# Kernel optimization log

Hardware: AMD Instinct MI355X
Metric: run time of the kernel (lower is better)

## Reference

```python
import jax, jax.numpy as jnp
import numpy as np

# Llama-2-7B-like GQA attention, prefill over packed equal-length sequences
H = 4096      # hidden_size
NH = 32       # num_attention_heads
NKV = 8       # num_key_value_heads
HD = H // NH  # head_dim = 128
B = 4         # number of packed sequences
S = 1024      # seq_len per sequence
T = B * S     # total packed tokens
BASE = 10000.0  # rope_theta


def setup_inputs() -> dict:
    key = jax.random.key(0)
    ks = jax.random.split(key, 5)
    x = jax.random.normal(ks[0], (T, H), jnp.float32)
    positions = jnp.tile(jnp.arange(S, dtype=jnp.int32), B)  # per-seq positions
    kv_cache = jnp.zeros((1,), jnp.float32)  # placeholder (prefill: kv from current tokens)
    init = 0.02
    wq = jax.random.normal(ks[1], (NH * HD, H), jnp.float32) * init
    wk = jax.random.normal(ks[2], (NKV * HD, H), jnp.float32) * init
    wv = jax.random.normal(ks[3], (NKV * HD, H), jnp.float32) * init
    wo = jax.random.normal(ks[4], (H, NH * HD), jnp.float32) * init
    return {"x": x, "positions": positions, "kv_cache": kv_cache,
            "wq": wq, "wk": wk, "wv": wv, "wo": wo, "seq_len": S}


def _rope(xh, cos_b, sin_b):
    # xh: [T, Hh, D]; cos_b/sin_b: [T, 1, D] (freqs repeat-interleaved by 2)
    half = xh.shape[-1] // 2
    x_rot = jnp.concatenate([-xh[..., half:], xh[..., :half]], axis=-1)
    return xh * cos_b + x_rot * sin_b


def reference(x, positions, kv_cache, wq, wk, wv, wo, seq_len):
    Tn = x.shape[0]
    q = (x @ wq.T).reshape(Tn, NH, HD)
    k = (x @ wk.T).reshape(Tn, NKV, HD)
    v = (x @ wv.T).reshape(Tn, NKV, HD)
    # GQA: repeat_interleave kv heads
    rep = NH // NKV
    k = jnp.repeat(k, rep, axis=1)
    v = jnp.repeat(v, rep, axis=1)
    # RoPE tables (faithful to _precompute_freqs/_rotary_embeddings)
    inv_freq = 1.0 / (BASE ** (jnp.arange(0, HD, 2, dtype=jnp.float32) / HD))
    t = jnp.arange(seq_len, dtype=jnp.float32)
    freqs = t[:, None] * inv_freq[None, :]            # [S, D/2]
    cos, sin = jnp.cos(freqs), jnp.sin(freqs)
    pos = jnp.clip(positions.astype(jnp.int32), 0, seq_len - 1)
    cos_b = jnp.repeat(cos[pos], 2, axis=-1)[:, None, :]  # [T,1,D]
    sin_b = jnp.repeat(sin[pos], 2, axis=-1)[:, None, :]
    q = _rope(q, cos_b, sin_b)
    k = _rope(k, cos_b, sin_b)
    # Paged attention (prefill): causal attention within each packed sequence
    Bn = Tn // seq_len
    qb = q.reshape(Bn, seq_len, NH, HD)
    kb = k.reshape(Bn, seq_len, NH, HD)
    vb = v.reshape(Bn, seq_len, NH, HD)
    scores = jnp.einsum('bqhd,bkhd->bhqk', qb, kb) * (HD ** -0.5)
    causal = jnp.tril(jnp.ones((seq_len, seq_len), bool))
    scores = jnp.where(causal[None, None], scores, -jnp.inf)
    probs = jax.nn.softmax(scores, axis=-1)
    out = jnp.einsum('bhqk,bkhd->bqhd', probs, vb).reshape(Tn, NH * HD)
    return out @ wo.T
```

## Files before the change

### kernel.cpp

```cpp
#include <hip/hip_runtime.h>
#include <hip/hip_bf16.h>
#include <math.h>

#define T_TOK 4096
#define HID   4096
#define NHQ   32
#define NKVH  8
#define HDIM  128
#define SEQ   1024
#define NBATCH 4

typedef __attribute__((ext_vector_type(8))) short bf16x8;
typedef __attribute__((ext_vector_type(4))) float f32x4;

__device__ __forceinline__ unsigned short f2bf(float f) {
  union { float f; unsigned int u; } x; x.f = f;
  unsigned int r = x.u + 0x7FFFu + ((x.u >> 16) & 1u);
  return (unsigned short)(r >> 16);
}

#define GLOAD_LDS16(gp, lp)                                                        \
  __builtin_amdgcn_global_load_lds(                                                \
      (__attribute__((address_space(1))) void*)(unsigned long long)(const void*)(gp), \
      (__attribute__((address_space(3))) void*)(unsigned long long)(const void*)(lp), \
      16, 0, 0)

__global__ __launch_bounds__(256) void cast_all_k(const float* __restrict__ x,
                                                  const float* __restrict__ wq,
                                                  const float* __restrict__ wk,
                                                  const float* __restrict__ wv,
                                                  const float* __restrict__ wo,
                                                  unsigned short* __restrict__ xb,
                                                  unsigned short* __restrict__ wqkv,
                                                  unsigned short* __restrict__ wob) {
  int i = blockIdx.x * 256 + threadIdx.x;
  const float* src; unsigned short* dst; int off;
  if (i < 4194304)       { src = x;  dst = xb;   off = i; }
  else if (i < 8388608)  { src = wq; dst = wqkv; off = i - 4194304; }
  else if (i < 9437184)  { src = wk; dst = wqkv + 16777216; off = i - 8388608; }
  else if (i < 10485760) { src = wv; dst = wqkv + 20971520; off = i - 9437184; }
  else                   { src = wo; dst = wob;  off = i - 10485760; }
  float4 f = ((const float4*)src)[off];
  ushort4 o;
  o.x = f2bf(f.x); o.y = f2bf(f.y); o.z = f2bf(f.z); o.w = f2bf(f.w);
  ((ushort4*)dst)[off] = o;
}

template<bool FUSED>
__global__ __launch_bounds__(512, 2) void gemm8(const unsigned short* __restrict__ A,
                                                const unsigned short* __restrict__ B,
                                                float* __restrict__ C,
                                                const int* __restrict__ pos,
                                                unsigned short* __restrict__ qr,
                                                unsigned short* __restrict__ kr,
                                                unsigned short* __restrict__ vbuf,
                                                int N, int K) {
  __shared__ unsigned short AL[2][16384];
  __shared__ unsigned short BL[4][8192];
  const int tid  = threadIdx.x;
  const int lane = tid & 63;
  const int wave = tid >> 6;
  const int m16  = lane & 15;
  const int quad = lane >> 4;
  const int wm   = wave >> 1;
  const int wn   = wave & 1;

  const int gx = gridDim.x;
  const int nwg = gx * gridDim.y;
  const int orig = blockIdx.y * gx + blockIdx.x;
  const int swz = (orig & 7) * (nwg >> 3) + (orig >> 3);
  const long rowBase = (long)(swz / gx) * 256;
  const long colBase = (long)(swz % gx) * 128;

  int aoff[2], boff[2];
#pragma unroll
  for (int ks = 0; ks < 2; ++ks) {
    int sx = ((ks * 4 + quad) ^ (m16 & 7)) * 8;
    aoff[ks] = (wm * 64 + m16) * 64 + sx;
    boff[ks] = (wn * 32 + m16) * 64 + sx;
  }

  const long Kl = K;
  const int sck = ((tid & 7) ^ ((tid >> 3) & 7)) * 8;
  const unsigned short* gA = A + (rowBase + (tid >> 3)) * Kl + sck;
  const unsigned short* gB = B + (colBase + (tid >> 3)) * Kl + sck;
  const int dofs = wave * 512;

#define STG_B(slot_, ko_) { GLOAD_LDS16(gB + (ko_),            &BL[slot_][dofs]);         \
                            GLOAD_LDS16(gB + (ko_) + 64 * Kl,  &BL[slot_][4096 + dofs]); }
#define STG_A(slot_, ko_) { GLOAD_LDS16(gA + (ko_),            &AL[slot_][dofs]);         \
                            GLOAD_LDS16(gA + (ko_) + 64 * Kl,  &AL[slot_][4096 + dofs]);  \
                            GLOAD_LDS16(gA + (ko_) + 128 * Kl, &AL[slot_][8192 + dofs]);  \
                            GLOAD_LDS16(gA + (ko_) + 192 * Kl, &AL[slot_][12288 + dofs]); }

  f32x4 acc[4][4] = {};

  STG_B(0, 0); STG_A(0, 0); STG_B(1, 64); STG_A(1, 64);
  asm volatile("s_waitcnt vmcnt(6)" ::: "memory");
  __builtin_amdgcn_s_barrier();

  for (int it = 0; it < 16; ++it) {
#pragma unroll
    for (int u = 0; u < 4; ++u) {
      const int X = it * 4 + u;
      const int kn = ((X + 2) & 63) << 6;
      bf16x8 af[4][2], bf01[2][2], bf23[2][2];

#pragma unroll
      for (int mf = 0; mf < 4; ++mf)
#pragma unroll
        for (int ks = 0; ks < 2; ++ks)
          af[mf][ks] = *(const bf16x8*)(&AL[u & 1][aoff[ks] + mf * 1024]);
#pragma unroll
      for (int nf = 0; nf < 2; ++nf)
#pragma unroll
        for (int ks = 0; ks < 2; ++ks)
          bf01[nf][ks] = *(const bf16x8*)(&BL[u][boff[ks] + nf * 1024]);
      STG_B((u + 2) & 3, kn);
      asm volatile("s_waitcnt lgkmcnt(8)" ::: "memory");
      __builtin_amdgcn_s_barrier();
      asm volatile("s_waitcnt lgkmcnt(0)" ::: "memory");
      __builtin_amdgcn_s_setprio(1);
#pragma unroll
      for (int mf = 0; mf < 4; ++mf)
#pragma unroll
        for (int nf = 0; nf < 2; ++nf)
#pragma unroll
          for (int ks = 0; ks < 2; ++ks)
            acc[mf][nf] = __builtin_amdgcn_mfma_f32_16x16x32_bf16(af[mf][ks], bf01[nf][ks], acc[mf][nf], 0, 0, 0);
      __builtin_amdgcn_s_setprio(0);
      __builtin_amdgcn_s_barrier();

#pragma unroll
      for (int nf = 0; nf < 2; ++nf)
#pragma unroll
        for (int ks = 0; ks < 2; ++ks)
          bf23[nf][ks] = *(const bf16x8*)(&BL[u][boff[ks] + nf * 1024 + 4096]);
      STG_A(u & 1, kn);
      __builtin_amdgcn_s_barrier();
      asm volatile("s_waitcnt lgkmcnt(0)" ::: "memory");
      __builtin_amdgcn_s_setprio(1);
#pragma unroll
      for (int mf = 0; mf < 4; ++mf)
#pragma unroll
        for (int nf = 0; nf < 2; ++nf)
#pragma unroll
          for (int ks = 0; ks < 2; ++ks)
            acc[mf][nf + 2] = __builtin_amdgcn_mfma_f32_16x16x32_bf16(af[mf][ks], bf23[nf][ks], acc[mf][nf + 2], 0, 0, 0);
      __builtin_amdgcn_s_setprio(0);
      asm volatile("s_waitcnt vmcnt(6)" ::: "memory");
      __builtin_amdgcn_s_barrier();
    }
  }

  if (!FUSED) {
#pragma unroll
    for (int mf = 0; mf < 4; ++mf)
#pragma unroll
      for (int nf = 0; nf < 4; ++nf) {
        long c = colBase + wn * 32 + (nf & 1) * 16 + (nf >> 1) * 64 + m16;
#pragma unroll
        for (int reg = 0; reg < 4; ++reg) {
          long row = rowBase + wm * 64 + mf * 16 + quad * 4 + reg;
          C[row * N + c] = acc[mf][nf][reg];
        }
      }
    return;
  }

  const int n0 = (int)colBase;
  unsigned short* dst;
  int rstride, colofs;
  bool dorope;
  if (n0 < 4096)       { dst = qr;   rstride = NHQ * HDIM;  colofs = n0;        dorope = true; }
  else if (n0 < 5120)  { dst = kr;   rstride = NKVH * HDIM; colofs = n0 - 4096; dorope = true; }
  else                 { dst = vbuf; rstride = NKVH * HDIM; colofs = n0 - 5120; dorope = false; }
  const float c0 = -13.287712379549449f / 64.0f;
  float fA[2], fB[2];
#pragma unroll
  for (int e = 0; e < 2; ++e) {
    int d = wn * 32 + e * 16 + m16;
    fA[e] = exp2f(c0 * (float)(d >> 1));
    fB[e] = exp2f(c0 * (float)((d >> 1) + 32));
  }
#pragma unroll
  for (int mf = 0; mf < 4; ++mf) {
#pragma unroll
    for (int reg = 0; reg < 4; ++reg) {
      int grow = (int)rowBase + wm * 64 + mf * 16 + quad * 4 + reg;
      unsigned short* drow = dst + (long)grow * rstride + colofs;
      if (dorope) {
        int p = pos[grow];
        p = p < 0 ? 0 : (p > SEQ - 1 ? SEQ - 1 : p);
        float pf = (float)p;
#pragma unroll
        for (int e = 0; e < 2; ++e) {
          int d = wn * 32 + e * 16 + m16;
          float lo = acc[mf][e][reg], hi = acc[mf][e + 2][reg];
          float s1, cc1, s2, cc2;
          __sincosf(pf * fA[e], &s1, &cc1);
          __sincosf(pf * fB[e], &s2, &cc2);
          drow[d]      = f2bf(lo * cc1 - hi * s1);
          drow[d + 64] = f2bf(hi * cc2 + lo * s2);
        }
      } else {
#pragma unroll
        for (int e = 0; e < 2; ++e) {
          int d = wn * 32 + e * 16 + m16;
          drow[d]      = f2bf(acc[mf][e][reg]);
          drow[d + 64] = f2bf(acc[mf][e + 2][reg]);
        }
      }
    }
  }
}

#define ATT_SCALE_L2 0.12754227022f
__global__ __launch_bounds__(256) void attn_k(const unsigned short* __restrict__ Qp,
                                              const unsigned short* __restrict__ Kp,
                                              const unsigned short* __restrict__ Vp,
                                              unsigned short* __restrict__ Op) {
  const int pr = blockIdx.x, h = blockIdx.y, b = blockIdx.z;
  const int kvh = h >> 2;
  const int tid = threadIdx.x, wave = tid >> 6, lane = tid & 63;
  const int m16 = lane & 15, quad = lane >> 4;

  __shared__ unsigned short Ks[64][128];
  __shared__ unsigned short Vt[128][64];
  __shared__ unsigned short Ps[4][32][64];

  for (int pass = 0; pass < 2; ++pass) {
    const int qt = pass ? pr : (7 - pr);
    const int qbase = qt * 128;
    const int wq_lo = qbase + wave * 32;

    bf16x8 qa[2][4];
#pragma unroll
    for (int i = 0; i < 2; ++i) {
      const unsigned short* qrow =
          Qp + (long)(b * SEQ + wq_lo + i * 16 + m16) * (NHQ * HDIM) + h * HDIM;
#pragma unroll
      for (int kk = 0; kk < 4; ++kk)
        qa[i][kk] = *(const bf16x8*)(qrow + kk * 32 + quad * 8);
    }

    f32x4 o[2][8] = {};
    float mrow[2][4], lrow[2][4];
#pragma unroll
    for (int i = 0; i < 2; ++i)
#pragma unroll
      for (int r = 0; r < 4; ++r) { mrow[i][r] = -1e30f; lrow[i][r] = 0.f; }

    const int nkt = qt * 2 + 2;
    for (int kt = 0; kt < nkt; ++kt) {
      __syncthreads();
      const unsigned short* Kbase =
          Kp + (long)(b * SEQ + kt * 64) * (NKVH * HDIM) + kvh * HDIM;
      const unsigned short* Vbase =
          Vp + (long)(b * SEQ + kt * 64) * (NKVH * HDIM) + kvh * HDIM;
#pragma unroll
      for (int it = 0; it < 4; ++it) {
        int c = it * 256 + tid;
        int row = c >> 4, psg = c & 15;
        int sg = (psg & 8) | ((psg & 7) ^ (row & 7));
        GLOAD_LDS16(Kbase + row * (NKVH * HDIM) + sg * 8,
                    ((unsigned short*)Ks) + (it * 256 + wave * 64) * 8);
      }
#pragma unroll
      for (int it = 0; it < 4; ++it) {
        int seg = it * 4 + wave;
        uint4 dv = *(const uint4*)(Vbase + lane * (NKVH * HDIM) + seg * 8);
        const unsigned short* pv = (const unsigned short*)&dv;
#pragma unroll
        for (int e = 0; e < 8; ++e) {
          int d = seg * 8 + e;
          Vt[d][((((lane >> 3) + d) & 7) * 8) + (lane & 7)] = pv[e];
        }
      }
      __syncthreads();

      const bool active = (kt * 64) <= (wq_lo + 31);
      if (active) {
        f32x4 s4[2][4] = {};
#pragma unroll
        for (int kk = 0; kk < 4; ++kk) {
          bf16x8 kbf[4];
#pragma unroll
          for (int j = 0; j < 4; ++j) {
            int row = j * 16 + m16;
            int cl = kk * 4 + quad;
            int ps = (cl & 8) | ((cl & 7) ^ (row & 7));
            kbf[j] = *(const bf16x8*)(&Ks[row][ps * 8]);
          }
#pragma unroll
          for (int i = 0; i < 2; ++i)
#pragma unroll
            for (int j = 0; j < 4; ++j)
              s4[i][j] = __builtin_amdgcn_mfma_f32_16x16x32_bf16(qa[i][kk], kbf[j], s4[i][j], 0, 0, 0);
        }
        const bool full = (kt * 64 + 63) <= wq_lo;
#pragma unroll
        for (int i = 0; i < 2; ++i) {
#pragma unroll
          for (int r = 0; r < 4; ++r) {
            const int qrow = i * 16 + quad * 4 + r;
            const int qi = qbase + wave * 32 + qrow;
            float v[4];
#pragma unroll
            for (int j = 0; j < 4; ++j) {
              v[j] = s4[i][j][r] * ATT_SCALE_L2;
              if (!full && (kt * 64 + j * 16 + m16 > qi)) v[j] = -1e30f;
            }
            float mx = fmaxf(fmaxf(v[0], v[1]), fmaxf(v[2], v[3]));
            mx = fmaxf(mx, __shfl_xor(mx, 1));
            mx = fmaxf(mx, __shfl_xor(mx, 2));
            mx = fmaxf(mx, __shfl_xor(mx, 4));
            mx = fmaxf(mx, __shfl_xor(mx, 8));
            float mold = mrow[i][r];
            float mnew = fmaxf(mold, mx);
            float alpha = exp2f(mold - mnew);
            float rs = 0.f;
#pragma unroll
            for (int j = 0; j < 4; ++j) {
              float pj = exp2f(v[j] - mnew);
              rs += pj;
              int col = j * 16 + m16;
              Ps[wave][qrow][((((col >> 3) + qrow) & 7) * 8) + (col & 7)] = f2bf(pj);
            }
            rs += __shfl_xor(rs, 1); rs += __shfl_xor(rs, 2);
            rs += __shfl_xor(rs, 4); rs += __shfl_xor(rs, 8);
            lrow[i][r] = lrow[i][r] * alpha + rs;
            mrow[i][r] = mnew;
#pragma unroll
            for (int n = 0; n < 8; ++n) o[i][n][r] *= alpha;
          }
        }
#pragma unroll
        for (int kk = 0; kk < 2; ++kk) {
          bf16x8 pa[2], vb[8];
#pragma unroll
          for (int i = 0; i < 2; ++i) {
            int row = i * 16 + m16;
            pa[i] = *(const bf16x8*)(&Ps[wave][row][(((kk * 4 + quad) + row) & 7) * 8]);
          }
#pragma unroll
          for (int n = 0; n < 8; ++n) {
            int row = n * 16 + m16;
            vb[n] = *(const bf16x8*)(&Vt[row][(((kk * 4 + quad) + row) & 7) * 8]);
          }
#pragma unroll
          for (int i = 0; i < 2; ++i)
#pragma unroll
            for (int n = 0; n < 8; ++n)
              o[i][n] = __builtin_amdgcn_mfma_f32_16x16x32_bf16(pa[i], vb[n], o[i][n], 0, 0, 0);
        }
      }
    }
#pragma unroll
    for (int i = 0; i < 2; ++i) {
#pragma unroll
      for (int r = 0; r < 4; ++r) {
        float inv = 1.0f / lrow[i][r];
        unsigned short* orow =
            Op + (long)(b * SEQ + wq_lo + i * 16 + quad * 4 + r) * (NHQ * HDIM) + h * HDIM;
#pragma unroll
        for (int n = 0; n < 8; ++n)
          orow[n * 16 + m16] = f2bf(o[i][n][r] * inv);
      }
    }
  }
}

extern "C" void kernel_launch(void* const* d_in, const int* in_sizes, int n_in,
                              void* d_out, int out_size, void* d_ws, size_t ws_size,
                              hipStream_t stream) {
  (void)in_sizes; (void)n_in; (void)out_size; (void)ws_size;
  const float* x  = (const float*)d_in[0];
  const int* pos  = (const int*)d_in[1];
  const float* wq = (const float*)d_in[3];
  const float* wk = (const float*)d_in[4];
  const float* wv = (const float*)d_in[5];
  const float* wo = (const float*)d_in[6];
  float* out = (float*)d_out;

  char* ws = (char*)d_ws;
  unsigned short* xb    = (unsigned short*)(ws);
  unsigned short* wqkv  = (unsigned short*)(ws + (32ll << 20));
  unsigned short* wob   = (unsigned short*)(ws + (80ll << 20));
  unsigned short* qr    = (unsigned short*)(ws + (112ll << 20));
  unsigned short* kr    = (unsigned short*)(ws + (144ll << 20));
  unsigned short* vb_   = (unsigned short*)(ws + (152ll << 20));
  unsigned short* ao    = (unsigned short*)(ws + (160ll << 20));

  cast_all_k<<<57344, 256, 0, stream>>>(x, wq, wk, wv, wo, xb, wqkv, wob);
  gemm8<true><<<dim3(48, 16), 512, 0, stream>>>(xb, wqkv, nullptr, pos, qr, kr, vb_, 6144, 4096);
  attn_k<<<dim3(4, 32, 4), 256, 0, stream>>>(qr, kr, vb_, ao);
  gemm8<false><<<dim3(32, 16), 512, 0, stream>>>(ao, wob, out, nullptr, nullptr, nullptr, nullptr, 4096, 4096);
}
```

Measured before the change: 754.0 us.

## Restructure GEMM pipelines to 3-stage buffers and double-buffer attention K/V

The templated GEMM is split into a QKV kernel with a triple-buffered, simplified K-loop and a separate output-projection kernel. The new output kernel uses 256x256 tiles with a K-step of 32 and a different LDS swizzle. The attention kernel now double-buffers K and V tiles, prefetching the next tile while computing the current one and raising wave priority around the MFMA sections. The aim is to hide global-load latency and cut barriers, at the cost of more LDS and registers, which may lower occupancy.

New measurement: 744.4 us. Within noise of the previous version (-1.3%).

```diff
diff --git a/kernel.cpp b/kernel.cpp
--- a/kernel.cpp
+++ b/kernel.cpp
@@ -46,17 +46,15 @@
   ((ushort4*)dst)[off] = o;
 }
 
-template<bool FUSED>
-__global__ __launch_bounds__(512, 2) void gemm8(const unsigned short* __restrict__ A,
-                                                const unsigned short* __restrict__ B,
-                                                float* __restrict__ C,
-                                                const int* __restrict__ pos,
-                                                unsigned short* __restrict__ qr,
-                                                unsigned short* __restrict__ kr,
-                                                unsigned short* __restrict__ vbuf,
-                                                int N, int K) {
-  __shared__ unsigned short AL[2][16384];
-  __shared__ unsigned short BL[4][8192];
+__global__ __launch_bounds__(512, 2) void gemm_qkv(const unsigned short* __restrict__ A,
+                                                   const unsigned short* __restrict__ B,
+                                                   const int* __restrict__ pos,
+                                                   unsigned short* __restrict__ qr,
+                                                   unsigned short* __restrict__ kr,
+                                                   unsigned short* __restrict__ vbuf) {
+  const int K = 4096, nt = 64;
+  __shared__ unsigned short AS[3][16384];
+  __shared__ unsigned short BS[3][8192];
   const int tid  = threadIdx.x;
   const int lane = tid & 63;
   const int wave = tid >> 6;
@@ -65,10 +63,9 @@
   const int wm   = wave >> 1;
   const int wn   = wave & 1;
 
-  const int gx = gridDim.x;
-  const int nwg = gx * gridDim.y;
+  const int gx = 48;
   const int orig = blockIdx.y * gx + blockIdx.x;
-  const int swz = (orig & 7) * (nwg >> 3) + (orig >> 3);
+  const int swz = (orig & 7) * 96 + (orig >> 3);
   const long rowBase = (long)(swz / gx) * 256;
   const long colBase = (long)(swz % gx) * 128;
 
@@ -86,86 +83,58 @@
   const unsigned short* gB = B + (colBase + (tid >> 3)) * Kl + sck;
   const int dofs = wave * 512;
 
-#define STG_B(slot_, ko_) { GLOAD_LDS16(gB + (ko_),            &BL[slot_][dofs]);         \
-                            GLOAD_LDS16(gB + (ko_) + 64 * Kl,  &BL[slot_][4096 + dofs]); }
-#define STG_A(slot_, ko_) { GLOAD_LDS16(gA + (ko_),            &AL[slot_][dofs]);         \
-                            GLOAD_LDS16(gA + (ko_) + 64 * Kl,  &AL[slot_][4096 + dofs]);  \
-                            GLOAD_LDS16(gA + (ko_) + 128 * Kl, &AL[slot_][8192 + dofs]);  \
-                            GLOAD_LDS16(gA + (ko_) + 192 * Kl, &AL[slot_][12288 + dofs]); }
+#define STG_B(slot_, ko_) { GLOAD_LDS16(gB + (ko_),            &BS[slot_][dofs]);         \
+                            GLOAD_LDS16(gB + (ko_) + 64 * Kl,  &BS[slot_][4096 + dofs]); }
+#define STG_A(slot_, ko_) { GLOAD_LDS16(gA + (ko_),            &AS[slot_][dofs]);         \
+                            GLOAD_LDS16(gA + (ko_) + 64 * Kl,  &AS[slot_][4096 + dofs]);  \
+                            GLOAD_LDS16(gA + (ko_) + 128 * Kl, &AS[slot_][8192 + dofs]);  \
+                            GLOAD_LDS16(gA + (ko_) + 192 * Kl, &AS[slot_][12288 + dofs]); }
 
   f32x4 acc[4][4] = {};
 
-  STG_B(0, 0); STG_A(0, 0); STG_B(1, 64); STG_A(1, 64);
+  STG_A(0, 0); STG_B(0, 0);
+  STG_A(1, 64); STG_B(1, 64);
   asm volatile("s_waitcnt vmcnt(6)" ::: "memory");
   __builtin_amdgcn_s_barrier();
 
-  for (int it = 0; it < 16; ++it) {
-#pragma unroll
-    for (int u = 0; u < 4; ++u) {
-      const int X = it * 4 + u;
-      const int kn = ((X + 2) & 63) << 6;
-      bf16x8 af[4][2], bf01[2][2], bf23[2][2];
-
-#pragma unroll
-      for (int mf = 0; mf < 4; ++mf)
-#pragma unroll
-        for (int ks = 0; ks < 2; ++ks)
-          af[mf][ks] = *(const bf16x8*)(&AL[u & 1][aoff[ks] + mf * 1024]);
-#pragma unroll
-      for (int nf = 0; nf < 2; ++nf)
-#pragma unroll
-        for (int ks = 0; ks < 2; ++ks)
-          bf01[nf][ks] = *(const bf16x8*)(&BL[u][boff[ks] + nf * 1024]);
-      STG_B((u + 2) & 3, kn);
-      asm volatile("s_waitcnt lgkmcnt(8)" ::: "memory");
-      __builtin_amdgcn_s_barrier();
-      asm volatile("s_waitcnt lgkmcnt(0)" ::: "memory");
-      __builtin_amdgcn_s_setprio(1);
-#pragma unroll
-      for (int mf = 0; mf < 4; ++mf)
-#pragma unroll
-        for (int nf = 0; nf < 2; ++nf)
-#pragma unroll
-          for (int ks = 0; ks < 2; ++ks)
-            acc[mf][nf] = __builtin_amdgcn_mfma_f32_16x16x32_bf16(af[mf][ks], bf01[nf][ks], acc[mf][nf], 0, 0, 0);
-      __builtin_amdgcn_s_setprio(0);
-      __builtin_amdgcn_s_barrier();
-
-#pragma unroll
-      for (int nf = 0; nf < 2; ++nf)
-#pragma unroll
-        for (int ks = 0; ks < 2; ++ks)
-          bf23[nf][ks] = *(const bf16x8*)(&BL[u][boff[ks] + nf * 1024 + 4096]);
-      STG_A(u & 1, kn);
-      __builtin_amdgcn_s_barrier();
-      asm volatile("s_waitcnt lgkmcnt(0)" ::: "memory");
-      __builtin_amdgcn_s_setprio(1);
-#pragma unroll
-      for (int mf = 0; mf < 4; ++mf)
-#pragma unroll
-        for (int nf = 0; nf < 2; ++nf)
-#pragma unroll
-          for (int ks = 0; ks < 2; ++ks)
-            acc[mf][nf + 2] = __builtin_amdgcn_mfma_f32_16x16x32_bf16(af[mf][ks], bf23[nf][ks], acc[mf][nf + 2], 0, 0, 0);
-      __builtin_amdgcn_s_setprio(0);
-      asm volatile("s_waitcnt vmcnt(6)" ::: "memory");
-      __builtin_amdgcn_s_barrier();
-    }
-  }
-
-  if (!FUSED) {
-#pragma unroll
-    for (int mf = 0; mf < 4; ++mf)
-#pragma unroll
-      for (int nf = 0; nf < 4; ++nf) {
-        long c = colBase + wn * 32 + (nf & 1) * 16 + (nf >> 1) * 64 + m16;
-#pragma unroll
-        for (int reg = 0; reg < 4; ++reg) {
-          long row = rowBase + wm * 64 + mf * 16 + quad * 4 + reg;
-          C[row * N + c] = acc[mf][nf][reg];
-        }
-      }
-    return;
+  for (int g = 0; g < 22; ++g) {
+#pragma unroll
+    for (int u = 0; u < 3; ++u) {
+      const int t = g * 3 + u;
+      if (t < nt) {
+        const bool doStage = (t + 2) < nt;
+        const long kn = (long)(t + 2) * 64;
+        bf16x8 af[4][2], bfr[4][2];
+#pragma unroll
+        for (int mf = 0; mf < 4; ++mf)
+          af[mf][0] = *(const bf16x8*)(&AS[u][aoff[0] + mf * 1024]);
+#pragma unroll
+        for (int nf = 0; nf < 4; ++nf)
+          bfr[nf][0] = *(const bf16x8*)(&BS[u][boff[0] + (nf & 1) * 1024 + (nf >> 1) * 4096]);
+        if (doStage) { STG_A((u + 2) % 3, kn); STG_B((u + 2) % 3, kn); }
+#pragma unroll
+        for (int mf = 0; mf < 4; ++mf)
+          af[mf][1] = *(const bf16x8*)(&AS[u][aoff[1] + mf * 1024]);
+#pragma unroll
+        for (int nf = 0; nf < 4; ++nf)
+          bfr[nf][1] = *(const bf16x8*)(&BS[u][boff[1] + (nf & 1) * 1024 + (nf >> 1) * 4096]);
+        __builtin_amdgcn_s_setprio(1);
+#pragma unroll
+        for (int mf = 0; mf < 4; ++mf)
+#pragma unroll
+          for (int nf = 0; nf < 4; ++nf)
+            acc[mf][nf] = __builtin_amdgcn_mfma_f32_16x16x32_bf16(af[mf][0], bfr[nf][0], acc[mf][nf], 0, 0, 0);
+#pragma unroll
+        for (int mf = 0; mf < 4; ++mf)
+#pragma unroll
+          for (int nf = 0; nf < 4; ++nf)
+            acc[mf][nf] = __builtin_amdgcn_mfma_f32_16x16x32_bf16(af[mf][1], bfr[nf][1], acc[mf][nf], 0, 0, 0);
+        __builtin_amdgcn_s_setprio(0);
+        if (doStage)        asm volatile("s_waitcnt vmcnt(6)" ::: "memory");
+        else if (t + 1 < nt) asm volatile("s_waitcnt vmcnt(0)" ::: "memory");
+        __builtin_amdgcn_s_barrier();
+      }
+    }
   }
 
   const int n0 = (int)colBase;
@@ -215,6 +184,100 @@
   }
 }
 
+__global__ __launch_bounds__(512, 2) void gemm_o(const unsigned short* __restrict__ A,
+                                                 const unsigned short* __restrict__ B,
+                                                 float* __restrict__ C) {
+  const int K = 4096, N = 4096, nt = 128;
+  __shared__ unsigned short AS[3][8192];
+  __shared__ unsigned short BS[3][8192];
+  const int tid  = threadIdx.x;
+  const int lane = tid & 63;
+  const int wave = tid >> 6;
+  const int m16  = lane & 15;
+  const int quad = lane >> 4;
+  const int wm   = wave >> 2;
+  const int wn   = wave & 3;
+
+  const int gx = 16;
+  const int orig = blockIdx.y * gx + blockIdx.x;
+  const int swz = (orig & 7) * 32 + (orig >> 3);
+  const long rowBase = (long)(swz / gx) * 256;
+  const long colBase = (long)(swz % gx) * 256;
+
+  const int slot8 = ((quad + 4 * (m16 & 1)) ^ (m16 >> 1)) * 8;
+  const int aob = (wm * 64 + (m16 >> 1)) * 64 + slot8;
+  const int bob = (wn * 32 + (m16 >> 1)) * 64 + slot8;
+
+  const long Kl = K;
+  const int z = (tid & 7) ^ ((tid >> 3) & 7);
+  const long srow = 2 * (tid >> 3) + (z >> 2);
+  const int sk = (z & 3) * 8;
+  const unsigned short* oA = A + (rowBase + srow) * Kl + sk;
+  const unsigned short* oB = B + (colBase + srow) * Kl + sk;
+  const int dofs = wave * 512;
+
+#define OSTG_A(sl_, ko_) { GLOAD_LDS16(oA + (ko_),            &AS[sl_][dofs]);         \
+                           GLOAD_LDS16(oA + (ko_) + 128 * Kl, &AS[sl_][4096 + dofs]); }
+#define OSTG_B(sl_, ko_) { GLOAD_LDS16(oB + (ko_),            &BS[sl_][dofs]);         \
+                           GLOAD_LDS16(oB + (ko_) + 128 * Kl, &BS[sl_][4096 + dofs]); }
+
+  f32x4 acc[8][4] = {};
+
+  OSTG_A(0, 0);  OSTG_B(0, 0);
+  OSTG_A(1, 32); OSTG_B(1, 32);
+  asm volatile("s_waitcnt vmcnt(4)" ::: "memory");
+  __builtin_amdgcn_s_barrier();
+
+  for (int g = 0; g < 43; ++g) {
+#pragma unroll
+    for (int u = 0; u < 3; ++u) {
+      const int t = g * 3 + u;
+      if (t < nt) {
+        const bool doStage = (t + 2) < nt;
+        const long kn = (long)(t + 2) * 32;
+        bf16x8 af[8], bfr[4];
+#pragma unroll
+        for (int nf = 0; nf < 4; ++nf)
+          bfr[nf] = *(const bf16x8*)(&BS[u][bob + nf * 512]);
+#pragma unroll
+        for (int mf = 0; mf < 4; ++mf)
+          af[mf] = *(const bf16x8*)(&AS[u][aob + mf * 512]);
+        if (doStage) { OSTG_A((u + 2) % 3, kn); OSTG_B((u + 2) % 3, kn); }
+#pragma unroll
+        for (int mf = 4; mf < 8; ++mf)
+          af[mf] = *(const bf16x8*)(&AS[u][aob + mf * 512]);
+        __builtin_amdgcn_s_setprio(1);
+#pragma unroll
+        for (int mf = 0; mf < 4; ++mf)
+#pragma unroll
+          for (int nf = 0; nf < 4; ++nf)
+            acc[mf][nf] = __builtin_amdgcn_mfma_f32_16x16x32_bf16(af[mf], bfr[nf], acc[mf][nf], 0, 0, 0);
+#pragma unroll
+        for (int mf = 4; mf < 8; ++mf)
+#pragma unroll
+          for (int nf = 0; nf < 4; ++nf)
+            acc[mf][nf] = __builtin_amdgcn_mfma_f32_16x16x32_bf16(af[mf], bfr[nf], acc[mf][nf], 0, 0, 0);
+        __builtin_amdgcn_s_setprio(0);
+        if (doStage)         asm volatile("s_waitcnt vmcnt(4)" ::: "memory");
+        else if (t + 1 < nt) asm volatile("s_waitcnt vmcnt(0)" ::: "memory");
+        __builtin_amdgcn_s_barrier();
+      }
+    }
+  }
+
+#pragma unroll
+  for (int mf = 0; mf < 8; ++mf)
+#pragma unroll
+    for (int nf = 0; nf < 4; ++nf) {
+      long c = colBase + wn * 64 + nf * 16 + m16;
+#pragma unroll
+      for (int reg = 0; reg < 4; ++reg) {
+        long row = rowBase + wm * 128 + mf * 16 + quad * 4 + reg;
+        C[row * N + c] = acc[mf][nf][reg];
+      }
+    }
+}
+
 #define ATT_SCALE_L2 0.12754227022f
 __global__ __launch_bounds__(256) void attn_k(const unsigned short* __restrict__ Qp,
                                               const unsigned short* __restrict__ Kp,
@@ -225,9 +288,38 @@
   const int tid = threadIdx.x, wave = tid >> 6, lane = tid & 63;
   const int m16 = lane & 15, quad = lane >> 4;
 
-  __shared__ unsigned short Ks[64][128];
-  __shared__ unsigned short Vt[128][64];
+  __shared__ unsigned short Ks[2][64][128];
+  __shared__ unsigned short Vt[2][128][64];
   __shared__ unsigned short Ps[4][32][64];
+
+  const unsigned short* Kh = Kp + (long)(b * SEQ) * (NKVH * HDIM) + kvh * HDIM;
+  const unsigned short* Vh = Vp + (long)(b * SEQ) * (NKVH * HDIM) + kvh * HDIM;
+
+#define STAGE_K(ktv, bufp) {                                               \
+    _Pragma("unroll")                                                      \
+    for (int it_ = 0; it_ < 4; ++it_) {                                    \
+      int c_ = it_ * 256 + tid;                                            \
+      int row_ = c_ >> 4, psg_ = c_ & 15;                                  \
+      int sg_ = (psg_ & 8) | ((psg_ & 7) ^ (row_ & 7));                    \
+      GLOAD_LDS16(Kh + ((long)(ktv) * 64 + row_) * (NKVH * HDIM) + sg_ * 8,\
+                  ((unsigned short*)(bufp)) + (it_ * 256 + wave * 64) * 8);\
+    } }
+
+#define LOAD_V(ktv, dvv) {                                                 \
+    _Pragma("unroll")                                                      \
+    for (int it_ = 0; it_ < 4; ++it_)                                      \
+      dvv[it_] = *(const uint4*)(Vh + ((long)(ktv) * 64 + lane) * (NKVH * HDIM) + (it_ * 4 + wave) * 8); }
+
+#define SCATTER_V(bufp, dvv) {                                             \
+    _Pragma("unroll")                                                      \
+    for (int it_ = 0; it_ < 4; ++it_) {                                    \
+      const unsigned short* pv_ = (const unsigned short*)&dvv[it_];        \
+      int seg_ = it_ * 4 + wave;                                           \
+      _Pragma("unroll")                                                    \
+      for (int e_ = 0; e_ < 8; ++e_) {                                     \
+        int d_ = seg_ * 8 + e_;                                            \
+        (bufp)[d_][((((lane >> 3) + d_) & 7) * 8) + (lane & 7)] = pv_[e_]; \
+      } } }
 
   for (int pass = 0; pass < 2; ++pass) {
     const int qt = pass ? pr : (7 - pr);
@@ -252,36 +344,24 @@
       for (int r = 0; r < 4; ++r) { mrow[i][r] = -1e30f; lrow[i][r] = 0.f; }
 
     const int nkt = qt * 2 + 2;
+
+    {
+      STAGE_K(0, Ks[0]);
+      uint4 dv[4];
+      LOAD_V(0, dv);
+      asm volatile("s_waitcnt vmcnt(0)" ::: "memory");
+      SCATTER_V(Vt[0], dv);
+    }
+    __syncthreads();
+
     for (int kt = 0; kt < nkt; ++kt) {
-      __syncthreads();
-      const unsigned short* Kbase =
-          Kp + (long)(b * SEQ + kt * 64) * (NKVH * HDIM) + kvh * HDIM;
-      const unsigned short* Vbase =
-          Vp + (long)(b * SEQ + kt * 64) * (NKVH * HDIM) + kvh * HDIM;
-#pragma unroll
-      for (int it = 0; it < 4; ++it) {
-        int c = it * 256 + tid;
-        int row = c >> 4, psg = c & 15;
-        int sg = (psg & 8) | ((psg & 7) ^ (row & 7));
-        GLOAD_LDS16(Kbase + row * (NKVH * HDIM) + sg * 8,
-                    ((unsigned short*)Ks) + (it * 256 + wave * 64) * 8);
-      }
-#pragma unroll
-      for (int it = 0; it < 4; ++it) {
-        int seg = it * 4 + wave;
-        uint4 dv = *(const uint4*)(Vbase + lane * (NKVH * HDIM) + seg * 8);
-        const unsigned short* pv = (const unsigned short*)&dv;
-#pragma unroll
-        for (int e = 0; e < 8; ++e) {
-          int d = seg * 8 + e;
-          Vt[d][((((lane >> 3) + d) & 7) * 8) + (lane & 7)] = pv[e];
-        }
-      }
-      __syncthreads();
-
+      const int cb = kt & 1;
       const bool active = (kt * 64) <= (wq_lo + 31);
+      const bool more = (kt + 1) < nkt;
+
+      f32x4 s4[2][4] = {};
       if (active) {
-        f32x4 s4[2][4] = {};
+        __builtin_amdgcn_s_setprio(1);
 #pragma unroll
         for (int kk = 0; kk < 4; ++kk) {
           bf16x8 kbf[4];
@@ -290,7 +370,7 @@
             int row = j * 16 + m16;
             int cl = kk * 4 + quad;
             int ps = (cl & 8) | ((cl & 7) ^ (row & 7));
-            kbf[j] = *(const bf16x8*)(&Ks[row][ps * 8]);
+            kbf[j] = *(const bf16x8*)(&Ks[cb][row][ps * 8]);
           }
 #pragma unroll
           for (int i = 0; i < 2; ++i)
@@ -298,6 +378,17 @@
             for (int j = 0; j < 4; ++j)
               s4[i][j] = __builtin_amdgcn_mfma_f32_16x16x32_bf16(qa[i][kk], kbf[j], s4[i][j], 0, 0, 0);
         }
+        __builtin_amdgcn_s_setprio(0);
+      }
+
+      uint4 dv[4];
+      if (more) {
+        STAGE_K(kt + 1, Ks[cb ^ 1]);
+        LOAD_V(kt + 1, dv);
+      }
+      asm volatile("" ::: "memory");
+
+      if (active) {
         const bool full = (kt * 64 + 63) <= wq_lo;
 #pragma unroll
         for (int i = 0; i < 2; ++i) {
@@ -335,6 +426,7 @@
             for (int n = 0; n < 8; ++n) o[i][n][r] *= alpha;
           }
         }
+        __builtin_amdgcn_s_setprio(1);
 #pragma unroll
         for (int kk = 0; kk < 2; ++kk) {
           bf16x8 pa[2], vb[8];
@@ -346,7 +438,7 @@
 #pragma unroll
           for (int n = 0; n < 8; ++n) {
             int row = n * 16 + m16;
-            vb[n] = *(const bf16x8*)(&Vt[row][(((kk * 4 + quad) + row) & 7) * 8]);
+            vb[n] = *(const bf16x8*)(&Vt[cb][row][(((kk * 4 + quad) + row) & 7) * 8]);
           }
 #pragma unroll
           for (int i = 0; i < 2; ++i)
@@ -354,8 +446,16 @@
             for (int n = 0; n < 8; ++n)
               o[i][n] = __builtin_amdgcn_mfma_f32_16x16x32_bf16(pa[i], vb[n], o[i][n], 0, 0, 0);
         }
-      }
-    }
+        __builtin_amdgcn_s_setprio(0);
+      }
+
+      if (more) {
+        asm volatile("s_waitcnt vmcnt(0)" ::: "memory");
+        SCATTER_V(Vt[cb ^ 1], dv);
+      }
+      __syncthreads();
+    }
+
 #pragma unroll
     for (int i = 0; i < 2; ++i) {
 #pragma unroll
@@ -393,7 +493,7 @@
   unsigned short* ao    = (unsigned short*)(ws + (160ll << 20));
 
   cast_all_k<<<57344, 256, 0, stream>>>(x, wq, wk, wv, wo, xb, wqkv, wob);
-  gemm8<true><<<dim3(48, 16), 512, 0, stream>>>(xb, wqkv, nullptr, pos, qr, kr, vb_, 6144, 4096);
+  gemm_qkv<<<dim3(48, 16), 512, 0, stream>>>(xb, wqkv, pos, qr, kr, vb_);
   attn_k<<<dim3(4, 32, 4), 256, 0, stream>>>(qr, kr, vb_, ao);
-  gemm8<false><<<dim3(32, 16), 512, 0, stream>>>(ao, wob, out, nullptr, nullptr, nullptr, nullptr, 4096, 4096);
-}
+  gemm_o<<<dim3(16, 16), 512, 0, stream>>>(ao, wob, out);
+}
```
